# Kernel optimization log

Hardware: AMD Instinct MI355X
Metric: run time of the kernel (lower is better)

Reference implementation:

```python
import jax, jax.numpy as jnp
import numpy as np

D_MODEL = 1024
NHEAD = 16
HEAD_DIM = D_MODEL // NHEAD
D_FF = 4096
EPS = 1e-5


def _layer_norm(x, g, b):
    mu = jnp.mean(x, axis=-1, keepdims=True)
    var = jnp.mean((x - mu) ** 2, axis=-1, keepdims=True)
    return (x - mu) * jax.lax.rsqrt(var + EPS) * g + b


def _rotate_every_two(x):
    x1 = x[..., ::2]
    x2 = x[..., 1::2]
    return jnp.stack([-x2, x1], axis=-1).reshape(x.shape)


def _rope_cos_sin(pos_start, length, head_dim, dtype):
    inv_freq = 1.0 / (10000.0 ** (jnp.arange(0, head_dim, 2, dtype=jnp.float32) / head_dim))
    pos = jnp.arange(pos_start, pos_start + length, dtype=jnp.float32)
    ang = jnp.einsum('i,j->ij', pos, inv_freq)  # (len, head_dim/2)
    cos = jnp.repeat(jnp.cos(ang), 2, axis=-1).astype(dtype)
    sin = jnp.repeat(jnp.sin(ang), 2, axis=-1).astype(dtype)
    return cos, sin


def setup_inputs() -> dict:
    key = jax.random.key(0)
    ks = jax.random.split(key, 16)
    s = 1.0 / np.sqrt(D_MODEL)
    sf = 1.0 / np.sqrt(D_FF)
    inp = {
        'src': jax.random.normal(ks[0], (2048, 2, D_MODEL), jnp.float32),
        'src_mask': jnp.ones((2048, 2048), jnp.float32),
        'Wq': jax.random.normal(ks[1], (D_MODEL, D_MODEL), jnp.float32) * s,
        'bq': jnp.zeros((D_MODEL,), jnp.float32),
        'Wk': jax.random.normal(ks[2], (D_MODEL, D_MODEL), jnp.float32) * s,
        'bk': jnp.zeros((D_MODEL,), jnp.float32),
        'Wv': jax.random.normal(ks[3], (D_MODEL, D_MODEL), jnp.float32) * s,
        'bv': jnp.zeros((D_MODEL,), jnp.float32),
        'Wo': jax.random.normal(ks[4], (D_MODEL, D_MODEL), jnp.float32) * s,
        'bo': jnp.zeros((D_MODEL,), jnp.float32),
        'W1': jax.random.normal(ks[5], (D_MODEL, D_FF), jnp.float32) * s,
        'b1': jnp.zeros((D_FF,), jnp.float32),
        'W2': jax.random.normal(ks[6], (D_FF, D_MODEL), jnp.float32) * sf,
        'b2': jnp.zeros((D_MODEL,), jnp.float32),
        'g1': jnp.ones((D_MODEL,), jnp.float32),
        'be1': jnp.zeros((D_MODEL,), jnp.float32),
        'g2': jnp.ones((D_MODEL,), jnp.float32),
        'be2': jnp.zeros((D_MODEL,), jnp.float32),
    }
    return inp


def _attention(q, k, v, attn_mask):
    # q, k, v: (S, B, D) already projected
    s, b, _ = q.shape
    kl = k.shape[0]

    def heads(x):
        # (L, B, D) -> (B, H, L, dh)
        return x.reshape(x.shape[0], b, NHEAD, HEAD_DIM).transpose(1, 2, 0, 3)

    qh, kh, vh = heads(q), heads(k), heads(v)
    q_cos, q_sin = _rope_cos_sin(0, s, HEAD_DIM, qh.dtype)
    k_cos, k_sin = _rope_cos_sin(0, kl, HEAD_DIM, kh.dtype)
    qh = qh * q_cos + _rotate_every_two(qh) * q_sin
    kh = kh * k_cos + _rotate_every_two(kh) * k_sin

    scores = jnp.einsum('bhqd,bhkd->bhqk', qh, kh) / np.sqrt(HEAD_DIM)
    if attn_mask is not None:
        scores = jnp.where(attn_mask[None, None, :, :] < 0.1, -jnp.inf, scores)
    w = jax.nn.softmax(scores, axis=-1)
    out = jnp.einsum('bhqk,bhkd->bhqd', w, vh)  # (B, H, S, dh)
    out = out.transpose(2, 0, 1, 3).reshape(s, b, D_MODEL)
    return out


def reference(src, src_mask, Wq, bq, Wk, bk, Wv, bv, Wo, bo, W1, b1, W2, b2, g1, be1, g2, be2):
    q = src @ Wq + bq
    k = src @ Wk + bk
    v = src @ Wv + bv
    attn = _attention(q, k, v, src_mask) @ Wo + bo
    src2 = _layer_norm(src + attn, g1, be1)
    ff = jax.nn.relu(src2 @ W1 + b1) @ W2 + b2
    out = _layer_norm(src2 + ff, g2, be2)
    return out
```

## Files before the change

kernel.cpp:

```cpp
#include <hip/hip_runtime.h>
#include <math.h>

#define S_LEN 2048
#define DM 1024
#define NH 16
#define HD 64
#define DFF 4096
#define MROWS 4096

typedef unsigned short u16;
typedef __attribute__((ext_vector_type(8))) __bf16 bf16x8;
typedef __attribute__((ext_vector_type(4))) float f32x4;
typedef __attribute__((ext_vector_type(16))) float f32x16;
typedef __attribute__((ext_vector_type(4))) int int32x4;

__device__ __forceinline__ u16 f2bf(float f) {
  unsigned u = __float_as_uint(f);
  unsigned r = (u + 0x7fffu + ((u >> 16) & 1u)) >> 16;
  return (u16)r;
}

__device__ __forceinline__ float bf2f(u16 u) {
  return __uint_as_float((unsigned)u << 16);
}

__device__ __forceinline__ unsigned cvtpk_bf16(float lo, float hi) {
  unsigned r;
  asm("v_cvt_pk_bf16_f32 %0, %1, %2" : "=v"(r) : "v"(lo), "v"(hi));
  return r;
}

__device__ __forceinline__ void gload_lds16(const void* g, void* l) {
  __builtin_amdgcn_global_load_lds((__attribute__((address_space(1))) void*)g,
                                   (__attribute__((address_space(3))) void*)l, 16, 0, 0);
}

__global__ __launch_bounds__(256) void k_transpose4(const float* __restrict__ W0, const float* __restrict__ W1,
                                                    const float* __restrict__ W2, const float* __restrict__ W3,
                                                    u16* __restrict__ T0, u16* __restrict__ T1,
                                                    u16* __restrict__ T2, u16* __restrict__ T3) {
  __shared__ float tile[32][33];
  const float* W = blockIdx.z == 0 ? W0 : blockIdx.z == 1 ? W1 : blockIdx.z == 2 ? W2 : W3;
  u16* Wt = blockIdx.z == 0 ? T0 : blockIdx.z == 1 ? T1 : blockIdx.z == 2 ? T2 : T3;
  int n0 = blockIdx.x * 32, k0 = blockIdx.y * 32;
  int tx = threadIdx.x & 31, ty = threadIdx.x >> 5;
  #pragma unroll
  for (int r = ty; r < 32; r += 8) tile[r][tx] = W[(size_t)(k0 + r) * 1024 + n0 + tx];
  __syncthreads();
  #pragma unroll
  for (int r = ty; r < 32; r += 8) Wt[(size_t)(n0 + r) * 1024 + k0 + tx] = f2bf(tile[tx][r]);
}

__global__ __launch_bounds__(256) void k_transpose_bf16(const float* __restrict__ W,
                                                        u16* __restrict__ Wt, int K, int N) {
  __shared__ float tile[32][33];
  int n0 = blockIdx.x * 32, k0 = blockIdx.y * 32;
  int tx = threadIdx.x & 31, ty = threadIdx.x >> 5;
  #pragma unroll
  for (int r = ty; r < 32; r += 8) tile[r][tx] = W[(size_t)(k0 + r) * N + n0 + tx];
  __syncthreads();
  #pragma unroll
  for (int r = ty; r < 32; r += 8) Wt[(size_t)(n0 + r) * K + k0 + tx] = f2bf(tile[tx][r]);
}

__global__ __launch_bounds__(256) void k_f2bf4(const float4* __restrict__ in,
                                               ushort4* __restrict__ out, int n4) {
  int i = blockIdx.x * 256 + threadIdx.x;
  if (i >= n4) return;
  float4 v = in[i];
  ushort4 o;
  o.x = f2bf(v.x); o.y = f2bf(v.y); o.z = f2bf(v.z); o.w = f2bf(v.w);
  out[i] = o;
}

__global__ __launch_bounds__(256) void k_rope_table(float* __restrict__ cosT,
                                                    float* __restrict__ sinT) {
  int idx = blockIdx.x * 256 + threadIdx.x;
  if (idx >= S_LEN * 32) return;
  int s = idx >> 5, i = idx & 31;
  float inv = powf(10000.f, -(float)(2 * i) / 64.f);
  float ang = (float)s * inv;
  cosT[idx] = cosf(ang);
  sinT[idx] = sinf(ang);
}

__global__ __launch_bounds__(256) void k_cat3(const float* __restrict__ a, const float* __restrict__ b,
                                              const float* __restrict__ c, float* __restrict__ o) {
  int i = blockIdx.x * 256 + threadIdx.x;
  if (i >= 3072) return;
  o[i] = i < 1024 ? a[i] : (i < 2048 ? b[i - 1024] : c[i - 2048]);
}

__global__ __launch_bounds__(256) void k_mask_flags(const float* __restrict__ mask,
                                                    unsigned char* __restrict__ flags) {
  int kt = blockIdx.x, qt = blockIdx.y;
  const float* mp = mask + (size_t)(qt * 64) * S_LEN + kt * 64;
  int tr = threadIdx.x >> 2;
  int tc = (threadIdx.x & 3) * 16;
  int ok = 1;
  #pragma unroll
  for (int c = 0; c < 16; c += 4) {
    float4 v = *(const float4*)(mp + (size_t)tr * S_LEN + tc + c);
    ok &= (v.x >= 0.1f) & (v.y >= 0.1f) & (v.z >= 0.1f) & (v.w >= 0.1f);
  }
  ok = __all(ok) ? 1 : 0;
  __shared__ int sh[4];
  if ((threadIdx.x & 63) == 0) sh[threadIdx.x >> 6] = ok;
  __syncthreads();
  if (threadIdx.x == 0) flags[qt * 32 + kt] = (sh[0] & sh[1] & sh[2] & sh[3]) ? 0 : 1;
}

enum { EPI_F32 = 0, EPI_RELU_BF16 = 2, EPI_PARTB = 4, EPI_BF16 = 5 };

template <int EPI>
__global__ __launch_bounds__(512, 2) void k_gemm256(const u16* __restrict__ A,
                                                    const u16* __restrict__ Bt,
                                                    const float* __restrict__ bias,
                                                    float* __restrict__ Cf, u16* __restrict__ Cb,
                                                    int M, int N, int K, int ldc, int Kc) {
  __shared__ __attribute__((aligned(16))) u16 As[4][256 * 32];
  __shared__ __attribute__((aligned(16))) u16 Bs[4][256 * 32];

  int nx = gridDim.x;
  int nwg = nx * gridDim.y;
  int flat = blockIdx.y * nx + blockIdx.x;
  int id = (flat & 7) * (nwg >> 3) + (flat >> 3);
  int n0 = (id % nx) * 256;
  int m0 = (id / nx) * 256;
  int kz = blockIdx.z * Kc;

  int tid = threadIdx.x;
  int lane = tid & 63, w = tid >> 6;
  int wm = (w >> 2) * 128, wn = (w & 3) * 64;
  int l15 = lane & 15, l4 = lane >> 4;
  int NT = Kc >> 5;

  const u16* aS[2];
  const u16* bS[2];
  int dslot[2];
  #pragma unroll
  for (int j = 0; j < 2; ++j) {
    int P = j * 512 + tid;
    int r = P >> 2;
    int sl = (P & 3) ^ (r & 3);
    aS[j] = A + (size_t)(m0 + r) * K + kz + sl * 8;
    bS[j] = Bt + (size_t)(n0 + r) * K + kz + sl * 8;
    dslot[j] = j * 512 + w * 64;
  }

  f32x4 acc[8][4] = {};

  #pragma unroll
  for (int t = 0; t < 3; ++t) {
    #pragma unroll
    for (int j = 0; j < 2; ++j) {
      gload_lds16(aS[j] + t * 32, &As[t][dslot[j] * 8]);
      gload_lds16(bS[j] + t * 32, &Bs[t][dslot[j] * 8]);
    }
  }

  for (int t = 0; t < NT; ++t) {
    int buf = t & 3;
    if (t < NT - 2) asm volatile("s_waitcnt vmcnt(8)" ::: "memory");
    else if (t == NT - 2) asm volatile("s_waitcnt vmcnt(4)" ::: "memory");
    else asm volatile("s_waitcnt vmcnt(0)" ::: "memory");
    __builtin_amdgcn_s_barrier();

    if (t + 3 < NT) {
      int tn = t + 3;
      int bn = tn & 3;
      #pragma unroll
      for (int j = 0; j < 2; ++j) {
        gload_lds16(aS[j] + tn * 32, &As[bn][dslot[j] * 8]);
        gload_lds16(bS[j] + tn * 32, &Bs[bn][dslot[j] * 8]);
      }
    }

    bf16x8 af[8], bq[4];
    #pragma unroll
    for (int m = 0; m < 8; ++m) {
      int r = wm + m * 16 + l15;
      af[m] = *(const bf16x8*)&As[buf][r * 32 + (l4 ^ (r & 3)) * 8];
    }
    #pragma unroll
    for (int n = 0; n < 4; ++n) {
      int r = wn + n * 16 + l15;
      bq[n] = *(const bf16x8*)&Bs[buf][r * 32 + (l4 ^ (r & 3)) * 8];
    }
    __builtin_amdgcn_s_setprio(1);
    #pragma unroll
    for (int m = 0; m < 8; ++m)
      #pragma unroll
      for (int n = 0; n < 4; ++n)
        acc[m][n] = __builtin_amdgcn_mfma_f32_16x16x32_bf16(af[m], bq[n], acc[m][n], 0, 0, 0);
    __builtin_amdgcn_s_setprio(0);
  }

  size_t zoff = (size_t)blockIdx.z * M * ldc;
  #pragma unroll
  for (int m = 0; m < 8; ++m) {
    #pragma unroll
    for (int n = 0; n < 4; ++n) {
      int col = n0 + wn + n * 16 + l15;
      float bv = (EPI == EPI_PARTB) ? 0.f : bias[col];
      #pragma unroll
      for (int r = 0; r < 4; ++r) {
        int row = m0 + wm + m * 16 + l4 * 4 + r;
        float v = acc[m][n][r] + bv;
        size_t o = (size_t)row * ldc + col;
        if (EPI == EPI_F32) Cf[o] = v;
        else if (EPI == EPI_RELU_BF16) Cb[o] = f2bf(fmaxf(v, 0.f));
        else if (EPI == EPI_BF16) Cb[o] = f2bf(v);
        else Cb[zoff + o] = f2bf(v);
      }
    }
  }
}

#define QSCALE 0.180336881f
__global__ __launch_bounds__(256) void k_rope_heads(const u16* __restrict__ QKVb,
                                                    const float* __restrict__ cosT,
                                                    const float* __restrict__ sinT,
                                                    u16* __restrict__ Qh, u16* __restrict__ Kh,
                                                    u16* __restrict__ Vt) {
  int idx = blockIdx.x * 256 + threadIdx.x;
  if (idx >= MROWS * 512) return;
  int m = idx >> 9, c2 = idx & 511;
  int h = c2 >> 5, i = c2 & 31, d = 2 * i;
  int s = m >> 1, b = m & 1;
  int bh = b * NH + h;
  size_t base = (size_t)m * 3072 + h * 64 + d;
  float q0 = bf2f(QKVb[base]), q1 = bf2f(QKVb[base + 1]);
  float k0 = bf2f(QKVb[base + 1024]), k1 = bf2f(QKVb[base + 1025]);
  float v0 = bf2f(QKVb[base + 2048]), v1 = bf2f(QKVb[base + 2049]);
  float c = cosT[s * 32 + i], sn = sinT[s * 32 + i];
  size_t ho = ((size_t)bh * S_LEN + s) * 64 + d;
  Qh[ho]     = f2bf((q0 * c - q1 * sn) * QSCALE);
  Qh[ho + 1] = f2bf((q1 * c + q0 * sn) * QSCALE);
  Kh[ho]     = f2bf(k0 * c - k1 * sn);
  Kh[ho + 1] = f2bf(k1 * c + k0 * sn);
  size_t vo = ((size_t)bh * 64 + d) * S_LEN + s;
  Vt[vo] = f2bf(v0);
  Vt[vo + S_LEN] = f2bf(v1);
}

__global__ __launch_bounds__(256) void k_attn(const u16* __restrict__ Qh, const u16* __restrict__ Kh,
                                              const u16* __restrict__ Vt,
                                              const float* __restrict__ mask,
                                              const unsigned char* __restrict__ flags,
                                              u16* __restrict__ Out) {
  __shared__ __attribute__((aligned(16))) u16 Ks[2][128 * 64];
  __shared__ __attribute__((aligned(16))) u16 Vs[2][64 * 128];
  int f = blockIdx.y * gridDim.x + blockIdx.x;
  int xcd = f & 7, ii = f >> 3;
  int bh = xcd * 4 + (ii >> 4);
  int q0 = (ii & 15) * 128;
  int b = bh >> 4, h = bh & 15;
  int tid = threadIdx.x, lane = tid & 63, w = tid >> 6;
  int l31 = lane & 31, l5 = lane >> 5;

  int qrow = q0 + w * 32 + l31;
  int qt = qrow >> 6;

  bf16x8 qf[4];
  {
    const u16* qp = Qh + ((size_t)bh * S_LEN + qrow) * 64 + l5 * 8;
    #pragma unroll
    for (int dc = 0; dc < 4; ++dc) qf[dc] = *(const bf16x8*)(qp + dc * 16);
  }

  const u16* Kbase = Kh + (size_t)bh * S_LEN * 64;
  const u16* Vbase = Vt + (size_t)bh * 64 * S_LEN;

  int ksid[4], vsid[4];
  const u16* kg[4];
  const u16* vg[4];
  #pragma unroll
  for (int i = 0; i < 4; ++i) {
    int sid = i * 256 + tid;
    ksid[i] = sid;
    int kr = sid >> 3, kslot = sid & 7;
    kg[i] = Kbase + (size_t)kr * 64 + (kslot ^ (kr & 7)) * 8;
    vsid[i] = sid;
    int vr = sid >> 4, vslot = sid & 15;
    vg[i] = Vbase + (size_t)vr * S_LEN + ((vslot ^ (vr & 15))) * 8;
  }

  float m_run = -1e30f, l_run = 0.f;
  f32x16 oA = {}, oB = {};

  const int NTILE = S_LEN / 128;
  #pragma unroll
  for (int i = 0; i < 4; ++i) {
    gload_lds16(kg[i], &Ks[0][ksid[i] * 8]);
    gload_lds16(vg[i], &Vs[0][vsid[i] * 8]);
  }

  for (int t = 0; t < NTILE; ++t) {
    int cur = t & 1;
    int kv0 = t * 128;
    asm volatile("s_waitcnt vmcnt(0)" ::: "memory");
    __builtin_amdgcn_s_barrier();
    if (t + 1 < NTILE) {
      int kvn = (t + 1) * 128;
      #pragma unroll
      for (int i = 0; i < 4; ++i) {
        gload_lds16(kg[i] + (size_t)kvn * 64, &Ks[cur ^ 1][ksid[i] * 8]);
        gload_lds16(vg[i] + kvn, &Vs[cur ^ 1][vsid[i] * 8]);
      }
    }

    #pragma unroll
    for (int ksub = 0; ksub < 2; ++ksub) {
      int koff = ksub * 64;
      f32x16 sA = {}, sB = {};
      #pragma unroll
      for (int dc = 0; dc < 4; ++dc) {
        int r0 = koff + l31;
        int r1 = koff + 32 + l31;
        int slot = (dc * 2 + l5) ^ (l31 & 7);
        bf16x8 ka0 = *(const bf16x8*)&Ks[cur][r0 * 64 + slot * 8];
        bf16x8 ka1 = *(const bf16x8*)&Ks[cur][r1 * 64 + slot * 8];
        sA = __builtin_amdgcn_mfma_f32_32x32x16_bf16(ka0, qf[dc], sA, 0, 0, 0);
        sB = __builtin_amdgcn_mfma_f32_32x32x16_bf16(ka1, qf[dc], sB, 0, 0, 0);
      }

      int fl = flags[qt * 32 + ((kv0 + koff) >> 6)];
      if (fl) {
        const float* mrow = mask + (size_t)qrow * S_LEN + kv0 + koff;
        #pragma unroll
        for (int r = 0; r < 16; ++r) {
          int key = (r & 3) + 8 * (r >> 2) + 4 * l5;
          if (mrow[key] < 0.1f) sA[r] = -1e30f;
          if (mrow[key + 32] < 0.1f) sB[r] = -1e30f;
        }
      }

      float pm = m_run;
      #pragma unroll
      for (int r = 0; r < 16; ++r) pm = fmaxf(pm, fmaxf(sA[r], sB[r]));
      pm = fmaxf(pm, __shfl_xor(pm, 32, 64));
      if (!__all(pm <= m_run + 8.f)) {
        float corr = __builtin_amdgcn_exp2f(m_run - pm);
        m_run = pm;
        l_run *= corr;
        #pragma unroll
        for (int r = 0; r < 16; ++r) { oA[r] *= corr; oB[r] *= corr; }
      }
      float ps = 0.f;
      #pragma unroll
      for (int r = 0; r < 16; ++r) {
        sA[r] = __builtin_amdgcn_exp2f(sA[r] - m_run);
        sB[r] = __builtin_amdgcn_exp2f(sB[r] - m_run);
        ps += sA[r] + sB[r];
      }
      l_run += ps;

      #pragma unroll
      for (int kh = 0; kh < 2; ++kh) {
        f32x16 s = kh ? sB : sA;
        #pragma unroll
        for (int c = 0; c < 2; ++c) {
          int base = c * 8;
          unsigned u0 = cvtpk_bf16(s[base + 0], s[base + 1]);
          unsigned u1 = cvtpk_bf16(s[base + 2], s[base + 3]);
          unsigned u2 = cvtpk_bf16(s[base + 4], s[base + 5]);
          unsigned u3 = cvtpk_bf16(s[base + 6], s[base + 7]);
          asm volatile("v_permlane32_swap_b32 %0, %1" : "+v"(u0), "+v"(u2));
          asm volatile("v_permlane32_swap_b32 %0, %1" : "+v"(u1), "+v"(u3));
          int32x4 wds = {(int)u0, (int)u1, (int)u2, (int)u3};
          bf16x8 pb = *(bf16x8*)&wds;
          int kslot = ksub * 8 + (kh * 2 + c) * 2 + l5;
          int vr0 = l31, vr1 = 32 + l31;
          bf16x8 va0 = *(const bf16x8*)&Vs[cur][vr0 * 128 + (kslot ^ (vr0 & 15)) * 8];
          bf16x8 va1 = *(const bf16x8*)&Vs[cur][vr1 * 128 + (kslot ^ (vr1 & 15)) * 8];
          oA = __builtin_amdgcn_mfma_f32_32x32x16_bf16(va0, pb, oA, 0, 0, 0);
          oB = __builtin_amdgcn_mfma_f32_32x32x16_bf16(va1, pb, oB, 0, 0, 0);
        }
      }
    }
  }

  float l_tot = l_run + __shfl_xor(l_run, 32, 64);
  float inv = 1.f / l_tot;
  int mrow = qrow * 2 + b;
  u16* op = Out + (size_t)mrow * DM + h * 64;
  #pragma unroll
  for (int db = 0; db < 2; ++db) {
    f32x16 o = db ? oB : oA;
    #pragma unroll
    for (int g = 0; g < 4; ++g) {
      int d0 = db * 32 + 8 * g + 4 * l5;
      ushort4 st;
      st.x = f2bf(o[4 * g + 0] * inv);
      st.y = f2bf(o[4 * g + 1] * inv);
      st.z = f2bf(o[4 * g + 2] * inv);
      st.w = f2bf(o[4 * g + 3] * inv);
      *(ushort4*)(op + d0) = st;
    }
  }
}

__device__ __forceinline__ float wave_sum(float v) {
  #pragma unroll
  for (int off = 32; off >= 1; off >>= 1) v += __shfl_xor(v, off, 64);
  return v;
}

template <int WB>
__global__ __launch_bounds__(256) void k_lnp(const u16* __restrict__ pb, const float* __restrict__ addf,
                                             const float* __restrict__ bvec,
                                             const float* __restrict__ gw, const float* __restrict__ bw,
                                             float* __restrict__ Yf, u16* __restrict__ Yb) {
  int m = blockIdx.x;
  int tid = threadIdx.x, lane = tid & 63, w = tid >> 6;
  __shared__ float part[4];
  __shared__ float shv[2];
  float4 sc = ((const float4*)(addf + (size_t)m * DM))[tid];
  float4 bv = ((const float4*)bvec)[tid];
  float vx = sc.x + bv.x, vy = sc.y + bv.y, vz = sc.z + bv.z, vw = sc.w + bv.w;
  #pragma unroll
  for (int z = 0; z < 4; ++z) {
    ushort4 qv = ((const ushort4*)(pb + (size_t)z * MROWS * DM + (size_t)m * DM))[tid];
    vx += bf2f(qv.x); vy += bf2f(qv.y); vz += bf2f(qv.z); vw += bf2f(qv.w);
  }
  float s = wave_sum(vx + vy + vz + vw);
  if (lane == 0) part[w] = s;
  __syncthreads();
  if (tid == 0) shv[0] = (part[0] + part[1] + part[2] + part[3]) * (1.f / DM);
  __syncthreads();
  float mu = shv[0];
  float d0 = vx - mu, d1 = vy - mu, d2 = vz - mu, d3 = vw - mu;
  float q = wave_sum(d0 * d0 + d1 * d1 + d2 * d2 + d3 * d3);
  if (lane == 0) part[w] = q;
  __syncthreads();
  if (tid == 0) shv[1] = rsqrtf((part[0] + part[1] + part[2] + part[3]) * (1.f / DM) + 1e-5f);
  __syncthreads();
  float rstd = shv[1];
  float4 g4 = ((const float4*)gw)[tid];
  float4 b4 = ((const float4*)bw)[tid];
  float y0 = d0 * rstd * g4.x + b4.x;
  float y1 = d1 * rstd * g4.y + b4.y;
  float y2 = d2 * rstd * g4.z + b4.z;
  float y3 = d3 * rstd * g4.w + b4.w;
  ((float4*)(Yf + (size_t)m * DM))[tid] = make_float4(y0, y1, y2, y3);
  if (WB) {
    ushort4 o;
    o.x = f2bf(y0); o.y = f2bf(y1); o.z = f2bf(y2); o.w = f2bf(y3);
    ((ushort4*)(Yb + (size_t)m * DM))[tid] = o;
  }
}

extern "C" void kernel_launch(void* const* d_in, const int* in_sizes, int n_in,
                              void* d_out, int out_size, void* d_ws, size_t ws_size,
                              hipStream_t stream) {
  (void)in_sizes; (void)n_in; (void)out_size; (void)ws_size;
  const float* src  = (const float*)d_in[0];
  const float* mask = (const float*)d_in[1];
  const float* Wq = (const float*)d_in[2];  const float* bq  = (const float*)d_in[3];
  const float* Wk = (const float*)d_in[4];  const float* bk  = (const float*)d_in[5];
  const float* Wv = (const float*)d_in[6];  const float* bv  = (const float*)d_in[7];
  const float* Wo = (const float*)d_in[8];  const float* bo  = (const float*)d_in[9];
  const float* W1 = (const float*)d_in[10]; const float* b1  = (const float*)d_in[11];
  const float* W2 = (const float*)d_in[12]; const float* b2  = (const float*)d_in[13];
  const float* g1 = (const float*)d_in[14]; const float* be1 = (const float*)d_in[15];
  const float* g2 = (const float*)d_in[16]; const float* be2 = (const float*)d_in[17];
  float* out = (float*)d_out;

  char* base = (char*)d_ws;
  size_t off = 0;
  auto carve = [&](size_t bytes) -> void* {
    void* r = base + off;
    off += (bytes + 255) & ~(size_t)255;
    return r;
  };
  u16* Wq_t = (u16*)carve(2ull * 1024 * 1024);
  u16* Wk_t = (u16*)carve(2ull * 1024 * 1024);
  u16* Wv_t = (u16*)carve(2ull * 1024 * 1024);
  u16* Wo_t = (u16*)carve(2ull * 1024 * 1024);
  u16* W1_t = (u16*)carve(2ull * 4096 * 1024);
  u16* W2_t = (u16*)carve(2ull * 1024 * 4096);
  u16* Xbf  = (u16*)carve(2ull * 4096 * 1024);
  float* cosT = (float*)carve(4ull * 2048 * 32);
  float* sinT = (float*)carve(4ull * 2048 * 32);
  float* bqkv = (float*)carve(4ull * 3072);
  unsigned char* mflags = (unsigned char*)carve(1024);
  u16* attn_out = (u16*)carve(2ull * 4096 * 1024);
  float* src2f = (float*)carve(4ull * 4096 * 1024);
  float* QKV = (float*)carve(4ull * 4096 * 3072);
  u16* Qh = (u16*)carve(2ull * 32 * 2048 * 64);
  u16* Kh = (u16*)carve(2ull * 32 * 2048 * 64);
  u16* Vt = (u16*)carve(2ull * 32 * 2048 * 64);
  u16* QKVb = (u16*)QKV;
  u16* woPb = (u16*)QKV;
  u16* ff1 = (u16*)QKV;
  u16* ffPb = (u16*)((char*)QKV + 32ull * 1024 * 1024);
  u16* src2b = (u16*)Vt;

  dim3 blk(256);
  dim3 blk5(512);
  k_transpose4<<<dim3(32, 32, 4), blk, 0, stream>>>(Wq, Wk, Wv, Wo, Wq_t, Wk_t, Wv_t, Wo_t);
  k_transpose_bf16<<<dim3(128, 32), blk, 0, stream>>>(W1, W1_t, 1024, 4096);
  k_transpose_bf16<<<dim3(32, 128), blk, 0, stream>>>(W2, W2_t, 4096, 1024);
  k_f2bf4<<<dim3(4096), blk, 0, stream>>>((const float4*)src, (ushort4*)Xbf, 4096 * 1024 / 4);
  k_rope_table<<<dim3(256), blk, 0, stream>>>(cosT, sinT);
  k_cat3<<<dim3(12), blk, 0, stream>>>(bq, bk, bv, bqkv);
  k_mask_flags<<<dim3(32, 32), blk, 0, stream>>>(mask, mflags);
  k_gemm256<EPI_BF16><<<dim3(12, 16, 1), blk5, 0, stream>>>(Xbf, Wq_t, bqkv, nullptr, QKVb, 4096, 3072, 1024, 3072, 1024);
  k_rope_heads<<<dim3(MROWS * 512 / 256), blk, 0, stream>>>(QKVb, cosT, sinT, Qh, Kh, Vt);
  k_attn<<<dim3(16, 32), blk, 0, stream>>>(Qh, Kh, Vt, mask, mflags, attn_out);
  k_gemm256<EPI_PARTB><<<dim3(4, 16, 4), blk5, 0, stream>>>(attn_out, Wo_t, nullptr, nullptr, woPb, 4096, 1024, 1024, 1024, 256);
  k_lnp<1><<<dim3(4096), blk, 0, stream>>>(woPb, src, bo, g1, be1, src2f, src2b);
  k_gemm256<EPI_RELU_BF16><<<dim3(16, 16, 1), blk5, 0, stream>>>(src2b, W1_t, b1, nullptr, ff1, 4096, 4096, 1024, 4096, 1024);
  k_gemm256<EPI_PARTB><<<dim3(4, 16, 4), blk5, 0, stream>>>(ff1, W2_t, nullptr, nullptr, ffPb, 4096, 1024, 4096, 1024, 1024);
  k_lnp<0><<<dim3(4096), blk, 0, stream>>>(ffPb, src2f, b2, g2, be2, out, nullptr);
}
```

Before: 302.3 us.

## Split attention KV range in two halves and merge partial softmax results

The attention kernel now divides the key/value sequence into two halves (split-K flash decoding style), doubling the grid to 1024 blocks. Each block writes an unnormalized partial output plus its running max and sum, and a new merge kernel combines the two halves and writes the final bf16 output. KV tiles shrink from 128 to 64 keys, which halves LDS use, and launch bounds now request 4 blocks per CU to raise occupancy. The cost is an extra kernel launch, an extra round trip of partial outputs through memory, and partials rounded to bf16 before they are merged.

```diff
diff --git a/kernel.cpp b/kernel.cpp
--- a/kernel.cpp
+++ b/kernel.cpp
@@ -244,18 +244,19 @@
   Vt[vo + S_LEN] = f2bf(v1);
 }
 
-__global__ __launch_bounds__(256) void k_attn(const u16* __restrict__ Qh, const u16* __restrict__ Kh,
-                                              const u16* __restrict__ Vt,
-                                              const float* __restrict__ mask,
-                                              const unsigned char* __restrict__ flags,
-                                              u16* __restrict__ Out) {
-  __shared__ __attribute__((aligned(16))) u16 Ks[2][128 * 64];
-  __shared__ __attribute__((aligned(16))) u16 Vs[2][64 * 128];
+__global__ __launch_bounds__(256, 4) void k_attn(const u16* __restrict__ Qh, const u16* __restrict__ Kh,
+                                                 const u16* __restrict__ Vt,
+                                                 const float* __restrict__ mask,
+                                                 const unsigned char* __restrict__ flags,
+                                                 u16* __restrict__ Oh, float2* __restrict__ ml) {
+  __shared__ __attribute__((aligned(16))) u16 Ks[2][64 * 64];
+  __shared__ __attribute__((aligned(16))) u16 Vs[2][64 * 64];
   int f = blockIdx.y * gridDim.x + blockIdx.x;
   int xcd = f & 7, ii = f >> 3;
-  int bh = xcd * 4 + (ii >> 4);
-  int q0 = (ii & 15) * 128;
-  int b = bh >> 4, h = bh & 15;
+  int bh = xcd * 4 + (ii >> 5);
+  int r5 = ii & 31;
+  int hf = r5 >> 4;
+  int q0 = (r5 & 15) * 128;
   int tid = threadIdx.x, lane = tid & 63, w = tid >> 6;
   int l31 = lane & 31, l5 = lane >> 5;
 
@@ -269,122 +270,111 @@
     for (int dc = 0; dc < 4; ++dc) qf[dc] = *(const bf16x8*)(qp + dc * 16);
   }
 
-  const u16* Kbase = Kh + (size_t)bh * S_LEN * 64;
-  const u16* Vbase = Vt + (size_t)bh * 64 * S_LEN;
-
-  int ksid[4], vsid[4];
-  const u16* kg[4];
-  const u16* vg[4];
-  #pragma unroll
-  for (int i = 0; i < 4; ++i) {
-    int sid = i * 256 + tid;
-    ksid[i] = sid;
-    int kr = sid >> 3, kslot = sid & 7;
-    kg[i] = Kbase + (size_t)kr * 64 + (kslot ^ (kr & 7)) * 8;
-    vsid[i] = sid;
-    int vr = sid >> 4, vslot = sid & 15;
-    vg[i] = Vbase + (size_t)vr * S_LEN + ((vslot ^ (vr & 15))) * 8;
+  const u16* KbaseH = Kh + ((size_t)bh * S_LEN + hf * 1024) * 64;
+  const u16* VbaseH = Vt + (size_t)bh * 64 * S_LEN + hf * 1024;
+  int koff[2], voff[2];
+  #pragma unroll
+  for (int i = 0; i < 2; ++i) {
+    int s = i * 256 + tid;
+    int kr = s >> 3, kslot = s & 7;
+    koff[i] = kr * 64 + (kslot ^ (kr & 7)) * 8;
+    int vr = s >> 3, vslot = s & 7;
+    voff[i] = vr * S_LEN + (vslot ^ (vr & 7)) * 8;
   }
 
   float m_run = -1e30f, l_run = 0.f;
   f32x16 oA = {}, oB = {};
 
-  const int NTILE = S_LEN / 128;
-  #pragma unroll
-  for (int i = 0; i < 4; ++i) {
-    gload_lds16(kg[i], &Ks[0][ksid[i] * 8]);
-    gload_lds16(vg[i], &Vs[0][vsid[i] * 8]);
-  }
-
-  for (int t = 0; t < NTILE; ++t) {
-    int cur = t & 1;
-    int kv0 = t * 128;
-    asm volatile("s_waitcnt vmcnt(0)" ::: "memory");
-    __builtin_amdgcn_s_barrier();
-    if (t + 1 < NTILE) {
-      int kvn = (t + 1) * 128;
-      #pragma unroll
-      for (int i = 0; i < 4; ++i) {
-        gload_lds16(kg[i] + (size_t)kvn * 64, &Ks[cur ^ 1][ksid[i] * 8]);
-        gload_lds16(vg[i] + kvn, &Vs[cur ^ 1][vsid[i] * 8]);
-      }
-    }
-
-    #pragma unroll
-    for (int ksub = 0; ksub < 2; ++ksub) {
-      int koff = ksub * 64;
-      f32x16 sA = {}, sB = {};
-      #pragma unroll
-      for (int dc = 0; dc < 4; ++dc) {
-        int r0 = koff + l31;
-        int r1 = koff + 32 + l31;
-        int slot = (dc * 2 + l5) ^ (l31 & 7);
-        bf16x8 ka0 = *(const bf16x8*)&Ks[cur][r0 * 64 + slot * 8];
-        bf16x8 ka1 = *(const bf16x8*)&Ks[cur][r1 * 64 + slot * 8];
-        sA = __builtin_amdgcn_mfma_f32_32x32x16_bf16(ka0, qf[dc], sA, 0, 0, 0);
-        sB = __builtin_amdgcn_mfma_f32_32x32x16_bf16(ka1, qf[dc], sB, 0, 0, 0);
-      }
-
-      int fl = flags[qt * 32 + ((kv0 + koff) >> 6)];
-      if (fl) {
-        const float* mrow = mask + (size_t)qrow * S_LEN + kv0 + koff;
-        #pragma unroll
-        for (int r = 0; r < 16; ++r) {
-          int key = (r & 3) + 8 * (r >> 2) + 4 * l5;
-          if (mrow[key] < 0.1f) sA[r] = -1e30f;
-          if (mrow[key + 32] < 0.1f) sB[r] = -1e30f;
-        }
-      }
-
-      float pm = m_run;
-      #pragma unroll
-      for (int r = 0; r < 16; ++r) pm = fmaxf(pm, fmaxf(sA[r], sB[r]));
-      pm = fmaxf(pm, __shfl_xor(pm, 32, 64));
-      if (!__all(pm <= m_run + 8.f)) {
-        float corr = __builtin_amdgcn_exp2f(m_run - pm);
-        m_run = pm;
-        l_run *= corr;
-        #pragma unroll
-        for (int r = 0; r < 16; ++r) { oA[r] *= corr; oB[r] *= corr; }
-      }
-      float ps = 0.f;
-      #pragma unroll
-      for (int r = 0; r < 16; ++r) {
-        sA[r] = __builtin_amdgcn_exp2f(sA[r] - m_run);
-        sB[r] = __builtin_amdgcn_exp2f(sB[r] - m_run);
-        ps += sA[r] + sB[r];
-      }
-      l_run += ps;
-
-      #pragma unroll
-      for (int kh = 0; kh < 2; ++kh) {
-        f32x16 s = kh ? sB : sA;
-        #pragma unroll
-        for (int c = 0; c < 2; ++c) {
-          int base = c * 8;
-          unsigned u0 = cvtpk_bf16(s[base + 0], s[base + 1]);
-          unsigned u1 = cvtpk_bf16(s[base + 2], s[base + 3]);
-          unsigned u2 = cvtpk_bf16(s[base + 4], s[base + 5]);
-          unsigned u3 = cvtpk_bf16(s[base + 6], s[base + 7]);
-          asm volatile("v_permlane32_swap_b32 %0, %1" : "+v"(u0), "+v"(u2));
-          asm volatile("v_permlane32_swap_b32 %0, %1" : "+v"(u1), "+v"(u3));
-          int32x4 wds = {(int)u0, (int)u1, (int)u2, (int)u3};
-          bf16x8 pb = *(bf16x8*)&wds;
-          int kslot = ksub * 8 + (kh * 2 + c) * 2 + l5;
-          int vr0 = l31, vr1 = 32 + l31;
-          bf16x8 va0 = *(const bf16x8*)&Vs[cur][vr0 * 128 + (kslot ^ (vr0 & 15)) * 8];
-          bf16x8 va1 = *(const bf16x8*)&Vs[cur][vr1 * 128 + (kslot ^ (vr1 & 15)) * 8];
-          oA = __builtin_amdgcn_mfma_f32_32x32x16_bf16(va0, pb, oA, 0, 0, 0);
-          oB = __builtin_amdgcn_mfma_f32_32x32x16_bf16(va1, pb, oB, 0, 0, 0);
-        }
-      }
-    }
-  }
+  #pragma unroll
+  for (int i = 0; i < 2; ++i) {
+    gload_lds16(KbaseH + koff[i], &Ks[0][(i * 256 + tid) * 8]);
+    gload_lds16(VbaseH + voff[i], &Vs[0][(i * 256 + tid) * 8]);
+  }
+
+#define ATTN_TILE(T, CUR)                                                                     \
+  do {                                                                                        \
+    asm volatile("s_waitcnt vmcnt(0)" ::: "memory");                                          \
+    __builtin_amdgcn_s_barrier();                                                             \
+    if ((T) + 1 < 16) {                                                                       \
+      const u16* kt_ = KbaseH + (size_t)((T) + 1) * 4096;                                     \
+      const u16* vt_ = VbaseH + ((T) + 1) * 64;                                               \
+      _Pragma("unroll")                                                                       \
+      for (int i = 0; i < 2; ++i) {                                                           \
+        gload_lds16(kt_ + koff[i], &Ks[(CUR) ^ 1][(i * 256 + tid) * 8]);                      \
+        gload_lds16(vt_ + voff[i], &Vs[(CUR) ^ 1][(i * 256 + tid) * 8]);                      \
+      }                                                                                       \
+    }                                                                                         \
+    f32x16 sA = {}, sB = {};                                                                  \
+    _Pragma("unroll")                                                                         \
+    for (int dc = 0; dc < 4; ++dc) {                                                          \
+      int r0 = l31, r1 = 32 + l31;                                                            \
+      bf16x8 ka0 = *(const bf16x8*)&Ks[CUR][r0 * 64 + (((dc * 2 + l5)) ^ (r0 & 7)) * 8];      \
+      bf16x8 ka1 = *(const bf16x8*)&Ks[CUR][r1 * 64 + (((dc * 2 + l5)) ^ (r1 & 7)) * 8];      \
+      sA = __builtin_amdgcn_mfma_f32_32x32x16_bf16(ka0, qf[dc], sA, 0, 0, 0);                 \
+      sB = __builtin_amdgcn_mfma_f32_32x32x16_bf16(ka1, qf[dc], sB, 0, 0, 0);                 \
+    }                                                                                         \
+    int kv0abs = hf * 1024 + (T) * 64;                                                        \
+    int fl = flags[qt * 32 + (kv0abs >> 6)];                                                  \
+    if (fl) {                                                                                 \
+      const float* mrow_ = mask + (size_t)qrow * S_LEN + kv0abs;                              \
+      _Pragma("unroll")                                                                       \
+      for (int r = 0; r < 16; ++r) {                                                          \
+        int key = (r & 3) + 8 * (r >> 2) + 4 * l5;                                            \
+        if (mrow_[key] < 0.1f) sA[r] = -1e30f;                                                \
+        if (mrow_[key + 32] < 0.1f) sB[r] = -1e30f;                                           \
+      }                                                                                       \
+    }                                                                                         \
+    float pm = m_run;                                                                         \
+    _Pragma("unroll")                                                                         \
+    for (int r = 0; r < 16; ++r) pm = fmaxf(pm, fmaxf(sA[r], sB[r]));                         \
+    pm = fmaxf(pm, __shfl_xor(pm, 32, 64));                                                   \
+    if (!__all(pm <= m_run + 8.f)) {                                                          \
+      float corr = __builtin_amdgcn_exp2f(m_run - pm);                                        \
+      m_run = pm;                                                                             \
+      l_run *= corr;                                                                          \
+      _Pragma("unroll")                                                                       \
+      for (int r = 0; r < 16; ++r) { oA[r] *= corr; oB[r] *= corr; }                          \
+    }                                                                                         \
+    float ps = 0.f;                                                                           \
+    _Pragma("unroll")                                                                         \
+    for (int r = 0; r < 16; ++r) {                                                            \
+      sA[r] = __builtin_amdgcn_exp2f(sA[r] - m_run);                                          \
+      sB[r] = __builtin_amdgcn_exp2f(sB[r] - m_run);                                          \
+      ps += sA[r] + sB[r];                                                                    \
+    }                                                                                         \
+    l_run += ps;                                                                              \
+    _Pragma("unroll")                                                                         \
+    for (int kh = 0; kh < 2; ++kh) {                                                          \
+      f32x16 s_ = kh ? sB : sA;                                                               \
+      _Pragma("unroll")                                                                       \
+      for (int c = 0; c < 2; ++c) {                                                           \
+        int base = c * 8;                                                                     \
+        unsigned u0 = cvtpk_bf16(s_[base + 0], s_[base + 1]);                                 \
+        unsigned u1 = cvtpk_bf16(s_[base + 2], s_[base + 3]);                                 \
+        unsigned u2 = cvtpk_bf16(s_[base + 4], s_[base + 5]);                                 \
+        unsigned u3 = cvtpk_bf16(s_[base + 6], s_[base + 7]);                                 \
+        asm volatile("v_permlane32_swap_b32 %0, %1" : "+v"(u0), "+v"(u2));                    \
+        asm volatile("v_permlane32_swap_b32 %0, %1" : "+v"(u1), "+v"(u3));                    \
+        int32x4 wds = {(int)u0, (int)u1, (int)u2, (int)u3};                                   \
+        bf16x8 pb = *(bf16x8*)&wds;                                                           \
+        int kslot = (kh * 2 + c) * 2 + l5;                                                    \
+        int vr0 = l31, vr1 = 32 + l31;                                                        \
+        bf16x8 va0 = *(const bf16x8*)&Vs[CUR][vr0 * 64 + (kslot ^ (vr0 & 7)) * 8];            \
+        bf16x8 va1 = *(const bf16x8*)&Vs[CUR][vr1 * 64 + (kslot ^ (vr1 & 7)) * 8];            \
+        oA = __builtin_amdgcn_mfma_f32_32x32x16_bf16(va0, pb, oA, 0, 0, 0);                   \
+        oB = __builtin_amdgcn_mfma_f32_32x32x16_bf16(va1, pb, oB, 0, 0, 0);                   \
+      }                                                                                       \
+    }                                                                                         \
+  } while (0)
+
+  for (int tt = 0; tt < 8; ++tt) {
+    ATTN_TILE(2 * tt, 0);
+    ATTN_TILE(2 * tt + 1, 1);
+  }
+#undef ATTN_TILE
 
   float l_tot = l_run + __shfl_xor(l_run, 32, 64);
-  float inv = 1.f / l_tot;
-  int mrow = qrow * 2 + b;
-  u16* op = Out + (size_t)mrow * DM + h * 64;
+  u16* op = Oh + (((size_t)hf * 32 + bh) * S_LEN + qrow) * 64;
   #pragma unroll
   for (int db = 0; db < 2; ++db) {
     f32x16 o = db ? oB : oA;
@@ -392,13 +382,48 @@
     for (int g = 0; g < 4; ++g) {
       int d0 = db * 32 + 8 * g + 4 * l5;
       ushort4 st;
-      st.x = f2bf(o[4 * g + 0] * inv);
-      st.y = f2bf(o[4 * g + 1] * inv);
-      st.z = f2bf(o[4 * g + 2] * inv);
-      st.w = f2bf(o[4 * g + 3] * inv);
+      st.x = f2bf(o[4 * g + 0]);
+      st.y = f2bf(o[4 * g + 1]);
+      st.z = f2bf(o[4 * g + 2]);
+      st.w = f2bf(o[4 * g + 3]);
       *(ushort4*)(op + d0) = st;
     }
   }
+  if (lane < 32) ml[((size_t)hf * 32 + bh) * S_LEN + qrow] = make_float2(m_run, l_tot);
+}
+
+__global__ __launch_bounds__(256) void k_attn_merge(const u16* __restrict__ Oh,
+                                                    const float2* __restrict__ ml,
+                                                    u16* __restrict__ Out) {
+  int idx = blockIdx.x * 256 + threadIdx.x;
+  int d8 = idx & 7;
+  int q = (idx >> 3) & 2047;
+  int bh = idx >> 14;
+  float2 a = ml[(size_t)bh * S_LEN + q];
+  float2 b = ml[(size_t)(32 + bh) * S_LEN + q];
+  float m = fmaxf(a.x, b.x);
+  float w0 = __builtin_amdgcn_exp2f(a.x - m);
+  float w1 = __builtin_amdgcn_exp2f(b.x - m);
+  float inv = 1.f / (a.y * w0 + b.y * w1);
+  w0 *= inv; w1 *= inv;
+  const ushort4* p0 = (const ushort4*)(Oh + ((size_t)bh * S_LEN + q) * 64 + d8 * 8);
+  const ushort4* p1 = (const ushort4*)(Oh + ((size_t)(32 + bh) * S_LEN + q) * 64 + d8 * 8);
+  ushort4 x0 = p0[0], x1 = p0[1];
+  ushort4 y0 = p1[0], y1 = p1[1];
+  int bb = bh >> 4, h = bh & 15;
+  int mrow = q * 2 + bb;
+  ushort4 o0, o1;
+  o0.x = f2bf(bf2f(x0.x) * w0 + bf2f(y0.x) * w1);
+  o0.y = f2bf(bf2f(x0.y) * w0 + bf2f(y0.y) * w1);
+  o0.z = f2bf(bf2f(x0.z) * w0 + bf2f(y0.z) * w1);
+  o0.w = f2bf(bf2f(x0.w) * w0 + bf2f(y0.w) * w1);
+  o1.x = f2bf(bf2f(x1.x) * w0 + bf2f(y1.x) * w1);
+  o1.y = f2bf(bf2f(x1.y) * w0 + bf2f(y1.y) * w1);
+  o1.z = f2bf(bf2f(x1.z) * w0 + bf2f(y1.z) * w1);
+  o1.w = f2bf(bf2f(x1.w) * w0 + bf2f(y1.w) * w1);
+  u16* op = Out + (size_t)mrow * DM + h * 64 + d8 * 8;
+  *(ushort4*)op = o0;
+  *(ushort4*)(op + 4) = o1;
 }
 
 __device__ __forceinline__ float wave_sum(float v) {
@@ -492,6 +517,8 @@
   u16* Kh = (u16*)carve(2ull * 32 * 2048 * 64);
   u16* Vt = (u16*)carve(2ull * 32 * 2048 * 64);
   u16* QKVb = (u16*)QKV;
+  u16* Oh   = (u16*)QKV;
+  float2* mlbuf = (float2*)((char*)QKV + 18ull * 1024 * 1024);
   u16* woPb = (u16*)QKV;
   u16* ff1 = (u16*)QKV;
   u16* ffPb = (u16*)((char*)QKV + 32ull * 1024 * 1024);
@@ -508,7 +535,8 @@
   k_mask_flags<<<dim3(32, 32), blk, 0, stream>>>(mask, mflags);
   k_gemm256<EPI_BF16><<<dim3(12, 16, 1), blk5, 0, stream>>>(Xbf, Wq_t, bqkv, nullptr, QKVb, 4096, 3072, 1024, 3072, 1024);
   k_rope_heads<<<dim3(MROWS * 512 / 256), blk, 0, stream>>>(QKVb, cosT, sinT, Qh, Kh, Vt);
-  k_attn<<<dim3(16, 32), blk, 0, stream>>>(Qh, Kh, Vt, mask, mflags, attn_out);
+  k_attn<<<dim3(32, 32), blk, 0, stream>>>(Qh, Kh, Vt, mask, mflags, Oh, mlbuf);
+  k_attn_merge<<<dim3(32 * 2048 * 8 / 256), blk, 0, stream>>>(Oh, mlbuf, attn_out);
   k_gemm256<EPI_PARTB><<<dim3(4, 16, 4), blk5, 0, stream>>>(attn_out, Wo_t, nullptr, nullptr, woPb, 4096, 1024, 1024, 1024, 256);
   k_lnp<1><<<dim3(4096), blk, 0, stream>>>(woPb, src, bo, g1, be1, src2f, src2b);
   k_gemm256<EPI_RELU_BF16><<<dim3(16, 16, 1), blk5, 0, stream>>>(src2b, W1_t, b1, nullptr, ff1, 4096, 4096, 1024, 4096, 1024);
```

New measurement: 346.2 us. +14.5%, slower.
